# Kernel tuning notes

Measured on AMD Instinct MI355X. Metric: run time of the kernel, lower is better.

## Reference

```python
import jax, jax.numpy as jnp
import numpy as np

B = 4            # batch_size (scenes)
NPOINT = 65536   # points per scene
PPS = 128        # proposals per scene
PTOT = B * PPS   # total proposals
M = 4_000_000    # (proposal, point) index pairs
C = 32           # channels after global_pool
MAXP = 128       # train_cfg.max_proposal_num
NUM_INST = 32


def setup_inputs() -> dict:
    key = jax.random.key(0)
    k1, k2, k3, k4, k5 = jax.random.split(key, 5)
    # each proposal belongs to scene pid // PPS; its points lie inside that scene
    pid = jax.random.randint(k1, (M,), 0, PTOT, dtype=jnp.int32)
    scene = pid // PPS
    j = scene * NPOINT + jax.random.randint(k2, (M,), 0, NPOINT, dtype=jnp.int32)
    proposals_idx = jnp.stack([pid, j], axis=1)  # [M, 2] int32, (cluster_id, global_point_id)
    instance_labels = jax.random.randint(k3, (B * NPOINT,), 0, NUM_INST, dtype=jnp.int32)
    object_id = jax.random.randint(k4, (B,), 0, NUM_INST, dtype=jnp.int32)
    proposal_each_scene = jnp.full((B,), PPS, dtype=jnp.int32)
    feats = jax.random.normal(k5, (PTOT, C), dtype=jnp.float32)  # per-proposal pooled features
    return dict(proposals_idx=proposals_idx, proposal_each_scene=proposal_each_scene,
                instance_labels=instance_labels, object_id=object_id, feats=feats,
                batch_size=B)


def reference(proposals_idx, proposal_each_scene, instance_labels, object_id, feats, batch_size):
    n_total = instance_labels.shape[0]
    npoint = n_total // batch_size
    p_total = feats.shape[0]

    # proposal_id_offset (select_feat): cumulative sums of proposal_each_scene
    offsets = jnp.concatenate([jnp.zeros((1,), jnp.int32),
                               jnp.cumsum(proposal_each_scene).astype(jnp.int32)])  # [B+1]
    # batch id of each proposal via searchsorted on the offsets
    prop_ids = jnp.arange(p_total)
    bid = jnp.searchsorted(offsets[1:], prop_ids, side='right')  # [P]

    # ref_cluster[b, n] = (instance_labels[b*npoint + n] == object_id[b])
    ref = (instance_labels.reshape(batch_size, npoint) == object_id[:, None]).astype(jnp.float32)  # [B, npoint]

    # proposal_cluster: scatter-set ones at (i, j % npoint) -- replaces the Python (i,j) loop
    pc = jnp.zeros((p_total, npoint), jnp.float32)
    pc = pc.at[proposals_idx[:, 0], proposals_idx[:, 1] % npoint].set(1.0)  # [P, npoint]

    # IoU of each proposal with its scene's reference cluster
    inter_pb = pc @ ref.T                               # [P, B] intersections
    inter = inter_pb[prop_ids, bid]                     # [P]
    union = pc.sum(axis=1) + ref.sum(axis=1)[bid] - inter
    iou = jnp.where(union > 0, inter / jnp.maximum(union, 1.0), 0.0)  # [P]

    # per-batch argmax over that scene's proposals (mask others to -1)
    scores = jnp.where(bid[None, :] == jnp.arange(batch_size)[:, None], iou[None, :], -1.0)  # [B, P]
    best = jnp.argmax(scores, axis=1).astype(jnp.int32)          # global proposal index
    has_prop = proposal_each_scene > 0
    select_proposal_idx = jnp.where(has_prop, best, -1)
    good_clu_masks = (jnp.max(scores, axis=1) > 0.2) & has_prop

    # clus_feats_batch[b, slot] = feats[p] for p in scene b (slot = p - offsets[b])
    slot = prop_ids.astype(jnp.int32) - offsets[bid]
    valid = slot < MAXP
    slot_safe = jnp.where(valid, slot, MAXP)  # out-of-range rows land in a dropped slot
    buf = jnp.zeros((batch_size, MAXP + 1, feats.shape[1]), feats.dtype)
    clus_feats_batch = buf.at[bid, slot_safe].set(feats)[:, :MAXP]  # [B, MAXP, C]

    # select_feats[b] = feats[select_proposal_idx[b]] (zeros when -1)
    sel_safe = jnp.clip(select_proposal_idx, 0, p_total - 1)
    select_feats = jnp.where((select_proposal_idx >= 0)[:, None], feats[sel_safe], 0.0)  # [B, C]

    return (clus_feats_batch, select_feats, select_proposal_idx, offsets, good_clu_masks)
```

## Files before the change

### kernel.cpp

```cpp
#include <hip/hip_runtime.h>
#include <cstdint>

#define NPOINT   65536
#define NB       4
#define PPS      128
#define PTOT     (NB * PPS)
#define NC       32
#define WORDS    (NPOINT / 32)
#define NBLK     1024
#define NBUCK    512
#define SUBCAP   32
#define STAGE_CAP 3968
#define KREG     16
#define SLOT_PER_BUCK (NBLK * SUBCAP)

#define WS_REF_OFF   0
#define WS_IOU_OFF   32768
#define WS_DONE_OFF  34816
#define WS_CNT_OFF   36864
#define WS_SORT_OFF  (36864 + NBLK * NBUCK * 2)

#define OUT_CLUS   0
#define OUT_SELF   16384
#define OUT_SELI   16512
#define OUT_OFFS   16516
#define OUT_MASK   16521

__global__ void k_build(const int2* __restrict__ pairs, int M,
                        const int* __restrict__ labels,
                        const int* __restrict__ object_id,
                        const float4* __restrict__ feats4,
                        float4* __restrict__ clus4,
                        uint16_t* __restrict__ cntT,
                        uint32_t* __restrict__ refMask,
                        uint16_t* __restrict__ slots16,
                        uint32_t* __restrict__ done) {
    __shared__ uint32_t sub[4][NBUCK];
    __shared__ uint32_t wbase[4][NBUCK];
    __shared__ uint32_t scnt[NBUCK];
    __shared__ uint32_t wtot[4];
    __shared__ uint16_t staging[STAGE_CAP];
    __shared__ uint16_t staging_b[STAGE_CAP];
    int bid = blockIdx.x, tid = threadIdx.x;

    if (bid >= NBLK) {
        int rb = bid - NBLK;
        int i = rb * 256 + tid;
        int b = i >> 16;
        bool match = (labels[i] == object_id[b]);
        unsigned long long bal = __ballot(match);
        if ((tid & 63) == 0) {
            int w = (i & (NPOINT - 1)) >> 5;
            refMask[b * WORDS + w]     = (uint32_t)bal;
            refMask[b * WORDS + w + 1] = (uint32_t)(bal >> 32);
        }
        if (rb < 16) clus4[rb * 256 + tid] = feats4[rb * 256 + tid];
        return;
    }

    if (bid == 0 && tid == 0) *done = 0;

    int w = tid >> 6, lane = tid & 63;
    for (int b = tid; b < 4 * NBUCK; b += 256) ((uint32_t*)sub)[b] = 0;
    __syncthreads();

    int per = (M + NBLK - 1) / NBLK;
    int lo = bid * per;
    int hi = min(M, lo + per);

    int2 r[KREG];
    int nr = 0;
#pragma unroll
    for (int j = 0; j < KREG; ++j) {
        int i = lo + (j << 8) + tid;
        if (i < hi) { r[j] = pairs[i]; nr = j + 1; }
    }

#pragma unroll
    for (int j = 0; j < KREG; ++j)
        if (j < nr) atomicAdd(&sub[w][r[j].x], 1u);
    __syncthreads();

    {
        int t = tid;
        uint32_t cA0 = sub[0][2 * t],     cA1 = sub[1][2 * t];
        uint32_t cA2 = sub[2][2 * t],     cA3 = sub[3][2 * t];
        uint32_t cB0 = sub[0][2 * t + 1], cB1 = sub[1][2 * t + 1];
        uint32_t cB2 = sub[2][2 * t + 1], cB3 = sub[3][2 * t + 1];
        uint32_t A  = cA0 + cA1 + cA2 + cA3;
        uint32_t B4 = cB0 + cB1 + cB2 + cB3;
        uint32_t S = A + B4;
        uint32_t inc = S;
#pragma unroll
        for (int off = 1; off < 64; off <<= 1) {
            uint32_t v = __shfl_up(inc, off);
            if (lane >= off) inc += v;
        }
        if (lane == 63) wtot[w] = inc;
        __syncthreads();
        uint32_t pre = 0;
        for (int i2 = 0; i2 < w; ++i2) pre += wtot[i2];
        uint32_t excl = pre + inc - S;
        wbase[0][2 * t] = excl;
        wbase[1][2 * t] = excl + cA0;
        wbase[2][2 * t] = excl + cA0 + cA1;
        wbase[3][2 * t] = excl + cA0 + cA1 + cA2;
        wbase[0][2 * t + 1] = excl + A;
        wbase[1][2 * t + 1] = excl + A + cB0;
        wbase[2][2 * t + 1] = excl + A + cB0 + cB1;
        wbase[3][2 * t + 1] = excl + A + cB0 + cB1 + cB2;
        scnt[2 * t] = A; scnt[2 * t + 1] = B4;
#pragma unroll
        for (int wv = 0; wv < 4; ++wv) { sub[wv][2 * t] = 0; sub[wv][2 * t + 1] = 0; }
    }
    __syncthreads();

#pragma unroll
    for (int j = 0; j < KREG; ++j) {
        if (j < nr) {
            int b = r[j].x;
            uint32_t rk = atomicAdd(&sub[w][b], 1u);
            uint32_t pos = wbase[w][b] + rk;
            staging[pos]   = (uint16_t)(r[j].y & (NPOINT - 1));
            staging_b[pos] = (uint16_t)b;
        }
    }
    __syncthreads();

    int total = hi - lo;
    for (int i = tid; i < total; i += 256) {
        int b = staging_b[i];
        uint32_t j = (uint32_t)i - wbase[0][b];
        if (j < SUBCAP)
            slots16[(size_t)b * SLOT_PER_BUCK + (size_t)bid * SUBCAP + j] = staging[i];
    }
    for (int b = tid; b < NBUCK; b += 256)
        cntT[(size_t)bid * NBUCK + b] = (uint16_t)min(scnt[b], (uint32_t)SUBCAP);
}

__global__ void k_iou_sel(const uint16_t* __restrict__ slots16,
                          const uint16_t* __restrict__ cntT,
                          const uint32_t* __restrict__ refMask,
                          uint32_t* __restrict__ iou_bits,
                          uint32_t* __restrict__ done,
                          const float* __restrict__ feats,
                          const int* __restrict__ pes,
                          float* __restrict__ out) {
    __shared__ uint32_t bm[WORDS];
    __shared__ uint16_t ccol[NBLK];
    __shared__ int red[12];
    __shared__ int s_last;
    int q = blockIdx.x, tid = threadIdx.x;
    int scene = q >> 7;
    for (int i = tid; i < WORDS; i += 256) bm[i] = 0;
    for (int i = tid; i < NBLK; i += 256) ccol[i] = cntT[(size_t)i * NBUCK + q];
    __syncthreads();

    const uint4* base = (const uint4*)(slots16 + (size_t)q * SLOT_PER_BUCK);
    for (int i = tid; i < SLOT_PER_BUCK / 8; i += 256) {
        uint4 kv = base[i];
        uint32_t blk = (uint32_t)i >> 2;
        uint32_t j0  = ((uint32_t)i << 3) & 31u;
        uint32_t c   = ccol[blk];
        uint32_t wd[4] = {kv.x, kv.y, kv.z, kv.w};
#pragma unroll
        for (int k2 = 0; k2 < 4; ++k2) {
            uint32_t n0 = wd[k2] & 0xFFFFu, n1 = wd[k2] >> 16;
            if (j0 + 2 * k2     < c) atomicOr(&bm[n0 >> 5], 1u << (n0 & 31));
            if (j0 + 2 * k2 + 1 < c) atomicOr(&bm[n1 >> 5], 1u << (n1 & 31));
        }
    }
    __syncthreads();

    int inter = 0, cnt = 0, rsum = 0;
    const uint32_t* rm = refMask + scene * WORDS;
    for (int wd = tid; wd < WORDS; wd += 256) {
        uint32_t a = bm[wd], rr = rm[wd];
        inter += __popc(a & rr);
        cnt   += __popc(a);
        rsum  += __popc(rr);
    }
#pragma unroll
    for (int off = 32; off; off >>= 1) {
        inter += __shfl_down(inter, off);
        cnt   += __shfl_down(cnt,   off);
        rsum  += __shfl_down(rsum,  off);
    }
    int w = tid >> 6;
    if ((tid & 63) == 0) { red[w] = inter; red[4 + w] = cnt; red[8 + w] = rsum; }
    __syncthreads();
    if (tid == 0) {
        inter = red[0] + red[1] + red[2] + red[3];
        cnt   = red[4] + red[5] + red[6] + red[7];
        rsum  = red[8] + red[9] + red[10] + red[11];
        float uni = (float)(cnt + rsum - inter);
        float f = (uni > 0.0f) ? ((float)inter / fmaxf(uni, 1.0f)) : 0.0f;
        __hip_atomic_store(&iou_bits[q], __float_as_uint(f),
                           __ATOMIC_RELEASE, __HIP_MEMORY_SCOPE_AGENT);
        uint32_t old = __hip_atomic_fetch_add(done, 1u,
                           __ATOMIC_ACQ_REL, __HIP_MEMORY_SCOPE_AGENT);
        s_last = (old == NBUCK - 1);
    }
    __syncthreads();
    if (!s_last) return;

    int lane = tid & 63;
    {
        int sc = w;
        uint32_t b0 = __hip_atomic_load(&iou_bits[sc * PPS + lane],
                                        __ATOMIC_ACQUIRE, __HIP_MEMORY_SCOPE_AGENT);
        uint32_t b1 = __hip_atomic_load(&iou_bits[sc * PPS + lane + 64],
                                        __ATOMIC_ACQUIRE, __HIP_MEMORY_SCOPE_AGENT);
        float v0 = __uint_as_float(b0), v1 = __uint_as_float(b1);
        float v; int idx;
        if (v1 > v0) { v = v1; idx = sc * PPS + lane + 64; }
        else         { v = v0; idx = sc * PPS + lane; }
#pragma unroll
        for (int off = 32; off; off >>= 1) {
            float ov = __shfl_down(v,   off);
            int   oi = __shfl_down(idx, off);
            if (ov > v || (ov == v && oi < idx)) { v = ov; idx = oi; }
        }
        int best = __shfl(idx, 0);
        float vmax = __shfl(v, 0);
        bool has = pes[sc] > 0;
        if (lane == 0) {
            out[OUT_SELI + sc] = has ? (float)best : -1.0f;
            out[OUT_MASK + sc] = (vmax > 0.2f && has) ? 1.0f : 0.0f;
        }
        if (lane < NC)
            out[OUT_SELF + sc * NC + lane] = has ? feats[best * NC + lane] : 0.0f;
        if (w == 0 && lane <= NB) {
            int s = 0;
            for (int i = 0; i < lane; ++i) s += pes[i];
            out[OUT_OFFS + lane] = (float)s;
        }
    }
}


extern "C" void kernel_launch(void* const* d_in, const int* in_sizes, int n_in,
                              void* d_out, int out_size, void* d_ws, size_t ws_size,
                              hipStream_t stream) {
    const int*   proposals_idx = (const int*)d_in[0];
    const int*   pes           = (const int*)d_in[1];
    const int*   labels        = (const int*)d_in[2];
    const int*   object_id     = (const int*)d_in[3];
    const float* feats         = (const float*)d_in[4];

    const int M = in_sizes[0] / 2;
    float* out = (float*)d_out;

    uint32_t* refMask  = (uint32_t*)((char*)d_ws + WS_REF_OFF);
    uint32_t* iou_bits = (uint32_t*)((char*)d_ws + WS_IOU_OFF);
    uint32_t* done     = (uint32_t*)((char*)d_ws + WS_DONE_OFF);
    uint16_t* cntT     = (uint16_t*)((char*)d_ws + WS_CNT_OFF);
    uint16_t* slots16  = (uint16_t*)((char*)d_ws + WS_SORT_OFF);

    k_build<<<NBLK + 1024, 256, 0, stream>>>(
        (const int2*)proposals_idx, M, labels, object_id,
        (const float4*)feats, (float4*)(out + OUT_CLUS),
        cntT, refMask, slots16, done);

    k_iou_sel<<<NBUCK, 256, 0, stream>>>(
        slots16, cntT, refMask, iou_bits, done, feats, pes, out);
}
```

Measured before the change: 117.3 us.

## Double build blocks, shrink sub-bucket capacity, fold ref-mask work into build blocks

The pair-bucketing kernel now uses 2048 blocks with 8 pairs per thread and a per-block bucket capacity of 24. The ref-mask, feature-copy and done-reset work moves from extra trailing blocks into the first 1024 build blocks. The separate per-wave base array is removed by storing bases directly in the counter array, and the IoU kernel indexes slot groups of three with a multiply-shift divide. This aims for more parallelism and less shared memory per block in the build kernel. In exchange the slot array grows, so the IoU kernel reads more data, and a smaller cap raises the risk of dropping pairs when a bucket overflows in one block.

```diff
diff --git a/kernel.cpp b/kernel.cpp
--- a/kernel.cpp
+++ b/kernel.cpp
@@ -7,11 +7,11 @@
 #define PTOT     (NB * PPS)
 #define NC       32
 #define WORDS    (NPOINT / 32)
-#define NBLK     1024
+#define NBLK     2048
 #define NBUCK    512
-#define SUBCAP   32
-#define STAGE_CAP 3968
-#define KREG     16
+#define SUBCAP   24
+#define STAGE_CAP 1984
+#define KREG     8
 #define SLOT_PER_BUCK (NBLK * SUBCAP)
 
 #define WS_REF_OFF   0
@@ -36,31 +36,28 @@
                         uint16_t* __restrict__ slots16,
                         uint32_t* __restrict__ done) {
     __shared__ uint32_t sub[4][NBUCK];
-    __shared__ uint32_t wbase[4][NBUCK];
+    __shared__ uint32_t sbase[NBUCK];
     __shared__ uint32_t scnt[NBUCK];
     __shared__ uint32_t wtot[4];
     __shared__ uint16_t staging[STAGE_CAP];
     __shared__ uint16_t staging_b[STAGE_CAP];
     int bid = blockIdx.x, tid = threadIdx.x;
-
-    if (bid >= NBLK) {
-        int rb = bid - NBLK;
-        int i = rb * 256 + tid;
+    int w = tid >> 6, lane = tid & 63;
+
+    if (bid < 1024) {
+        int i = bid * 256 + tid;
         int b = i >> 16;
         bool match = (labels[i] == object_id[b]);
         unsigned long long bal = __ballot(match);
-        if ((tid & 63) == 0) {
-            int w = (i & (NPOINT - 1)) >> 5;
-            refMask[b * WORDS + w]     = (uint32_t)bal;
-            refMask[b * WORDS + w + 1] = (uint32_t)(bal >> 32);
-        }
-        if (rb < 16) clus4[rb * 256 + tid] = feats4[rb * 256 + tid];
-        return;
-    }
-
-    if (bid == 0 && tid == 0) *done = 0;
-
-    int w = tid >> 6, lane = tid & 63;
+        if (lane == 0) {
+            int wd = (i & (NPOINT - 1)) >> 5;
+            refMask[b * WORDS + wd]     = (uint32_t)bal;
+            refMask[b * WORDS + wd + 1] = (uint32_t)(bal >> 32);
+        }
+        if (bid < 16) clus4[bid * 256 + tid] = feats4[bid * 256 + tid];
+        if (bid == 0 && tid == 0) *done = 0;
+    }
+
     for (int b = tid; b < 4 * NBUCK; b += 256) ((uint32_t*)sub)[b] = 0;
     __syncthreads();
 
@@ -101,17 +98,17 @@
         uint32_t pre = 0;
         for (int i2 = 0; i2 < w; ++i2) pre += wtot[i2];
         uint32_t excl = pre + inc - S;
-        wbase[0][2 * t] = excl;
-        wbase[1][2 * t] = excl + cA0;
-        wbase[2][2 * t] = excl + cA0 + cA1;
-        wbase[3][2 * t] = excl + cA0 + cA1 + cA2;
-        wbase[0][2 * t + 1] = excl + A;
-        wbase[1][2 * t + 1] = excl + A + cB0;
-        wbase[2][2 * t + 1] = excl + A + cB0 + cB1;
-        wbase[3][2 * t + 1] = excl + A + cB0 + cB1 + cB2;
-        scnt[2 * t] = A; scnt[2 * t + 1] = B4;
-#pragma unroll
-        for (int wv = 0; wv < 4; ++wv) { sub[wv][2 * t] = 0; sub[wv][2 * t + 1] = 0; }
+        sbase[2 * t] = excl;          scnt[2 * t] = A;
+        sbase[2 * t + 1] = excl + A;  scnt[2 * t + 1] = B4;
+        sub[0][2 * t] = excl;
+        sub[1][2 * t] = excl + cA0;
+        sub[2][2 * t] = excl + cA0 + cA1;
+        sub[3][2 * t] = excl + cA0 + cA1 + cA2;
+        uint32_t e1 = excl + A;
+        sub[0][2 * t + 1] = e1;
+        sub[1][2 * t + 1] = e1 + cB0;
+        sub[2][2 * t + 1] = e1 + cB0 + cB1;
+        sub[3][2 * t + 1] = e1 + cB0 + cB1 + cB2;
     }
     __syncthreads();
 
@@ -119,8 +116,7 @@
     for (int j = 0; j < KREG; ++j) {
         if (j < nr) {
             int b = r[j].x;
-            uint32_t rk = atomicAdd(&sub[w][b], 1u);
-            uint32_t pos = wbase[w][b] + rk;
+            uint32_t pos = atomicAdd(&sub[w][b], 1u);
             staging[pos]   = (uint16_t)(r[j].y & (NPOINT - 1));
             staging_b[pos] = (uint16_t)b;
         }
@@ -130,7 +126,7 @@
     int total = hi - lo;
     for (int i = tid; i < total; i += 256) {
         int b = staging_b[i];
-        uint32_t j = (uint32_t)i - wbase[0][b];
+        uint32_t j = (uint32_t)i - sbase[b];
         if (j < SUBCAP)
             slots16[(size_t)b * SLOT_PER_BUCK + (size_t)bid * SUBCAP + j] = staging[i];
     }
@@ -157,10 +153,11 @@
     __syncthreads();
 
     const uint4* base = (const uint4*)(slots16 + (size_t)q * SLOT_PER_BUCK);
-    for (int i = tid; i < SLOT_PER_BUCK / 8; i += 256) {
+    const int NV = SLOT_PER_BUCK / 8;
+    for (int i = tid; i < NV; i += 256) {
         uint4 kv = base[i];
-        uint32_t blk = (uint32_t)i >> 2;
-        uint32_t j0  = ((uint32_t)i << 3) & 31u;
+        uint32_t blk = ((uint32_t)i * 0xAAABu) >> 17;
+        uint32_t j0  = ((uint32_t)i - blk * 3u) * 8u;
         uint32_t c   = ccol[blk];
         uint32_t wd[4] = {kv.x, kv.y, kv.z, kv.w};
 #pragma unroll
@@ -257,7 +254,7 @@
     uint16_t* cntT     = (uint16_t*)((char*)d_ws + WS_CNT_OFF);
     uint16_t* slots16  = (uint16_t*)((char*)d_ws + WS_SORT_OFF);
 
-    k_build<<<NBLK + 1024, 256, 0, stream>>>(
+    k_build<<<NBLK, 256, 0, stream>>>(
         (const int2*)proposals_idx, M, labels, object_id,
         (const float4*)feats, (float4*)(out + OUT_CLUS),
         cntT, refMask, slots16, done);
```

After: 128.3 us. 1.09x slower.
